# Optimization experiments

Measured on AMD Instinct MI355X. Metric: run time of the kernel, lower is better.

The kernel has to match this reference:

```python
import jax, jax.numpy as jnp
import numpy as np

B, N, D = 4, 1024, 1024      # batch, seq_len, query_dim
H, DH = 16, 64               # heads, dim_head; inner = H*DH = 1024
INNER = H * DH
SCALE = DH ** -0.5


def setup_inputs() -> dict:
    key = jax.random.key(0)
    ks = jax.random.split(key, 8)
    x = jax.random.normal(ks[0], (B, N, D), dtype=jnp.float32)
    rel_pos = jax.random.normal(ks[1], (B * H, N, N), dtype=jnp.float32)
    query_mask = jax.random.randint(ks[2], (B, N), 0, 2).astype(bool)
    context_mask = jax.random.randint(ks[3], (B, N), 0, 2).astype(bool)
    # Linear weights stored (in, out); to_q/to_kv have no bias, to_out has bias.
    Wq = jax.random.normal(ks[4], (D, INNER), dtype=jnp.float32) / np.sqrt(D)
    Wkv = jax.random.normal(ks[5], (D, 2 * INNER), dtype=jnp.float32) / np.sqrt(D)
    Wo = jax.random.normal(ks[6], (INNER, D), dtype=jnp.float32) / np.sqrt(INNER)
    bo = jax.random.normal(ks[7], (D,), dtype=jnp.float32) * 0.01
    return {"x": x, "rel_pos": rel_pos, "query_mask": query_mask,
            "context_mask": context_mask, "Wq": Wq, "Wkv": Wkv, "Wo": Wo, "bo": bo}


def reference(x, rel_pos, query_mask, context_mask, Wq, Wkv, Wo, bo):
    # Self-attention (context = x)
    q = x @ Wq                                 # [B, N, INNER]
    kv = x @ Wkv                               # [B, N, 2*INNER]
    k, v = jnp.split(kv, 2, axis=-1)
    # (b n (h d)) -> (b h n d)
    split_heads = lambda t: t.reshape(B, N, H, DH).transpose(0, 2, 1, 3)
    q, k, v = map(split_heads, (q, k, v))
    sim = jnp.einsum('bhid,bhjd->bhij', q, k) * SCALE
    sim = sim + rel_pos.reshape(B, H, N, N)
    neg = -jnp.finfo(sim.dtype).max
    # query_mask: (b i) -> mask rows; context_mask: (b j) -> mask cols
    sim = jnp.where(query_mask[:, None, :, None], sim, neg)
    sim = jnp.where(context_mask[:, None, None, :], sim, neg)
    attn = jax.nn.softmax(sim, axis=-1)
    out = jnp.einsum('bhij,bhjd->bhid', attn, v)    # [B, H, N, DH]
    out = out.transpose(0, 2, 1, 3).reshape(B, N, INNER)
    return out @ Wo + bo
```

## Files before the change

### kernel.cpp

```cpp
#include <hip/hip_runtime.h>


#define NEGMAX 3.402823466e+38f

typedef short short8 __attribute__((ext_vector_type(8)));
typedef float f32x4 __attribute__((ext_vector_type(4)));

__device__ __forceinline__ unsigned short f2bf(float f) {
  unsigned int u = __float_as_uint(f);
  u += 0x7FFFu + ((u >> 16) & 1u);
  return (unsigned short)(u >> 16);
}

__device__ __forceinline__ void stage16(const void* g, void* lds_base, int lane) {
#if __has_builtin(__builtin_amdgcn_global_load_lds)
  __builtin_amdgcn_global_load_lds(
      (const __attribute__((address_space(1))) unsigned int*)g,
      (__attribute__((address_space(3))) unsigned int*)lds_base, 16, 0, 0);
#else
  *(int4*)((char*)lds_base + lane * 16) = *(const int4*)g;
#endif
}

__global__ void cast_x_k(const float* __restrict__ x, unsigned short* __restrict__ xb) {
  int i = (blockIdx.x * 256 + threadIdx.x) * 4;
  float4 v = *(const float4*)(x + i);
  ushort4 o;
  o.x = f2bf(v.x); o.y = f2bf(v.y); o.z = f2bf(v.z); o.w = f2bf(v.w);
  *(ushort4*)(xb + i) = o;
}

__global__ __launch_bounds__(256) void tcast_k(const float* __restrict__ src, int ldsrc,
                                               unsigned short* __restrict__ dst) {
  __shared__ float T[64][65];
  const int n0 = blockIdx.x * 64, d0 = blockIdx.y * 64;
  const int tx = threadIdx.x & 63, ty = threadIdx.x >> 6;
#pragma unroll
  for (int k = 0; k < 16; ++k) {
    int dl = k * 4 + ty;
    T[dl][tx] = src[(size_t)(d0 + dl) * ldsrc + n0 + tx];
  }
  __syncthreads();
#pragma unroll
  for (int k = 0; k < 16; ++k) {
    int nl = k * 4 + ty;
    dst[(size_t)(n0 + nl) * 1024 + d0 + tx] = f2bf(T[tx][nl]);
  }
}

template <int MODE>
__global__ __launch_bounds__(256) void gemm_bt_k(
    const unsigned short* __restrict__ A, const unsigned short* __restrict__ Bt,
    unsigned short* __restrict__ qws, unsigned short* __restrict__ kws,
    unsigned short* __restrict__ vtws,
    const float* __restrict__ bias, float* __restrict__ Cout) {
  constexpr int K = 1024;
  constexpr int NKB = K / 32;
  __shared__ alignas(16) unsigned short As[128 * 32];
  __shared__ alignas(16) unsigned short Bs[128 * 32];
  const int tid = threadIdx.x;
  const int lane = tid & 63, w = tid >> 6;
  const int quad = lane >> 4, lanelo = lane & 15;
  const int tRow = blockIdx.y * 128, tCol = blockIdx.x * 128;
  const int wr = (w >> 1) * 64, wc = (w & 1) * 64;
  const char* AgB = (const char*)(A + (size_t)tRow * K);
  const char* BgB = (const char*)(Bt + (size_t)tCol * K);
  const int c0 = tid, c1 = tid + 256;
  const size_t a0off = (size_t)(c0 >> 2) * 2048 + (c0 & 3) * 16;
  const size_t a1off = (size_t)(c1 >> 2) * 2048 + (c1 & 3) * 16;
  char* ldsA0 = (char*)As + w * 1024;
  char* ldsA1 = (char*)As + 4096 + w * 1024;
  char* ldsB0 = (char*)Bs + w * 1024;
  char* ldsB1 = (char*)Bs + 4096 + w * 1024;

  f32x4 acc[4][4];
#pragma unroll
  for (int i = 0; i < 4; ++i)
#pragma unroll
    for (int j = 0; j < 4; ++j) acc[i][j] = (f32x4){0.f, 0.f, 0.f, 0.f};

  for (int kb = 0; kb < NKB; ++kb) {
    if (kb) __syncthreads();
    const size_t ko = (size_t)kb * 64;
    stage16(AgB + a0off + ko, ldsA0, lane);
    stage16(AgB + a1off + ko, ldsA1, lane);
    stage16(BgB + a0off + ko, ldsB0, lane);
    stage16(BgB + a1off + ko, ldsB1, lane);
    __syncthreads();

    short8 af[4], bf[4];
#pragma unroll
    for (int i = 0; i < 4; ++i)
      af[i] = *(const short8*)(As + (wr + i * 16 + lanelo) * 32 + quad * 8);
#pragma unroll
    for (int j = 0; j < 4; ++j)
      bf[j] = *(const short8*)(Bs + (wc + j * 16 + lanelo) * 32 + quad * 8);
#pragma unroll
    for (int i = 0; i < 4; ++i)
#pragma unroll
      for (int j = 0; j < 4; ++j)
        acc[i][j] = __builtin_amdgcn_mfma_f32_16x16x32_bf16(af[i], bf[j], acc[i][j], 0, 0, 0);
  }

  if (MODE == 0) {
#pragma unroll
    for (int i = 0; i < 4; ++i) {
      int row = tRow + wr + i * 16 + quad * 4;
      int b_ = row >> 10;
      int npos = row & 1023;
#pragma unroll
      for (int j = 0; j < 4; ++j) {
        int col = tCol + wc + j * 16 + lanelo;
        if (col < 2048) {
          unsigned short* dst = (col < 1024) ? qws : kws;
          int c = col & 1023;
          int hh = c >> 6, dh = c & 63;
          size_t base = ((size_t)(b_ * 16 + hh) * 1024 + npos) * 64 + dh;
#pragma unroll
          for (int r = 0; r < 4; ++r) dst[base + (size_t)r * 64] = f2bf(acc[i][j][r]);
        } else {
          int c = col - 2048;
          ushort4 pk;
          pk.x = f2bf(acc[i][j][0]);
          pk.y = f2bf(acc[i][j][1]);
          pk.z = f2bf(acc[i][j][2]);
          pk.w = f2bf(acc[i][j][3]);
          *(ushort4*)&vtws[((size_t)(b_ * 16 + (c >> 6)) * 64 + (c & 63)) * 1024 + npos] = pk;
        }
      }
    }
  } else {
#pragma unroll
    for (int i = 0; i < 4; ++i) {
      int row = tRow + wr + i * 16 + quad * 4;
#pragma unroll
      for (int j = 0; j < 4; ++j) {
        int col = tCol + wc + j * 16 + lanelo;
        float bv = bias[col];
#pragma unroll
        for (int r = 0; r < 4; ++r)
          Cout[(size_t)(row + r) * 1024 + col] = acc[i][j][r] + bv;
      }
    }
  }
}

__global__ __launch_bounds__(64) void attn_k(
    const unsigned short* __restrict__ q_ws, const unsigned short* __restrict__ k_ws,
    const unsigned short* __restrict__ vt_ws, const float* __restrict__ rel,
    const int* __restrict__ qmask, const int* __restrict__ cmask,
    unsigned short* __restrict__ aout) {
  constexpr float SCALE = 0.125f;
  __shared__ alignas(16) unsigned short Pl[16 * 72];

  const int lane = threadIdx.x;
  const int quad = lane >> 4, lanelo = lane & 15;
  const int bh = blockIdx.y, b_ = bh >> 4, h = bh & 15;
  const int qrow0 = blockIdx.x * 16;

  const unsigned short* qg = q_ws + ((size_t)bh * 1024 + qrow0) * 64;
  short8 qf0 = *(const short8*)(qg + lanelo * 64 + quad * 8);
  short8 qf1 = *(const short8*)(qg + lanelo * 64 + 32 + quad * 8);

  float qmv[4];
#pragma unroll
  for (int r = 0; r < 4; ++r)
    qmv[r] = (qmask[b_ * 1024 + qrow0 + quad * 4 + r] != 0) ? 1.f : 0.f;

  const unsigned short* kg = k_ws + (size_t)bh * 65536;
  const unsigned short* vg = vt_ws + (size_t)bh * 65536;
  const float* relg = rel + ((size_t)bh * 1024 + qrow0) * 1024;
  const int* cmg = cmask + b_ * 1024;

  f32x4 o[4];
#pragma unroll
  for (int g = 0; g < 4; ++g) o[g] = (f32x4){0.f, 0.f, 0.f, 0.f};
  float m_run[4], l_run[4];
#pragma unroll
  for (int r = 0; r < 4; ++r) { m_run[r] = -NEGMAX; l_run[r] = 0.f; }

  float rl[4][4], cmv[4];
#pragma unroll
  for (int r = 0; r < 4; ++r)
#pragma unroll
    for (int c = 0; c < 4; ++c)
      rl[r][c] = relg[(size_t)(quad * 4 + r) * 1024 + c * 16 + lanelo];
#pragma unroll
  for (int c = 0; c < 4; ++c) cmv[c] = (cmg[c * 16 + lanelo] != 0) ? 1.f : 0.f;

  for (int kb = 0; kb < 16; ++kb) {
    const int ko = kb * 64;

    short8 kf0[4], kf1[4];
#pragma unroll
    for (int c = 0; c < 4; ++c) {
      const unsigned short* kr = kg + (size_t)(ko + c * 16 + lanelo) * 64 + quad * 8;
      kf0[c] = *(const short8*)(kr);
      kf1[c] = *(const short8*)(kr + 32);
    }
    short8 vf[4][2];
#pragma unroll
    for (int g = 0; g < 4; ++g)
#pragma unroll
      for (int c2 = 0; c2 < 2; ++c2)
        vf[g][c2] = *(const short8*)(vg + (size_t)(g * 16 + lanelo) * 1024 + ko + c2 * 32 + quad * 8);

    f32x4 s[4];
#pragma unroll
    for (int c = 0; c < 4; ++c) {
      s[c] = (f32x4){0.f, 0.f, 0.f, 0.f};
      s[c] = __builtin_amdgcn_mfma_f32_16x16x32_bf16(qf0, kf0[c], s[c], 0, 0, 0);
      s[c] = __builtin_amdgcn_mfma_f32_16x16x32_bf16(qf1, kf1[c], s[c], 0, 0, 0);
    }

    float rn[4][4], cn[4];
    if (kb + 1 < 16) {
#pragma unroll
      for (int r = 0; r < 4; ++r)
#pragma unroll
        for (int c = 0; c < 4; ++c)
          rn[r][c] = relg[(size_t)(quad * 4 + r) * 1024 + ko + 64 + c * 16 + lanelo];
#pragma unroll
      for (int c = 0; c < 4; ++c) cn[c] = (cmg[ko + 64 + c * 16 + lanelo] != 0) ? 1.f : 0.f;
    }

#pragma unroll
    for (int r = 0; r < 4; ++r) {
      const bool qok = qmv[r] != 0.f;
      float x[4], mloc = -NEGMAX;
#pragma unroll
      for (int c = 0; c < 4; ++c) {
        x[c] = (qok && cmv[c] != 0.f) ? s[c][r] * SCALE + rl[r][c] : -NEGMAX;
        mloc = fmaxf(mloc, x[c]);
      }
      for (int off = 1; off < 16; off <<= 1) mloc = fmaxf(mloc, __shfl_xor(mloc, off));
      float mnew = fmaxf(m_run[r], mloc);
      float alpha = __expf(m_run[r] - mnew);
      m_run[r] = mnew;
      float ps = 0.f;
      unsigned short pb[4];
#pragma unroll
      for (int c = 0; c < 4; ++c) {
        float p = __expf(x[c] - mnew);
        ps += p;
        pb[c] = f2bf(p);
      }
      for (int off = 1; off < 16; off <<= 1) ps += __shfl_xor(ps, off);
      l_run[r] = l_run[r] * alpha + ps;
#pragma unroll
      for (int g = 0; g < 4; ++g) o[g][r] *= alpha;
#pragma unroll
      for (int c = 0; c < 4; ++c) Pl[(quad * 4 + r) * 72 + c * 16 + lanelo] = pb[c];
    }

    if (kb + 1 < 16) {
#pragma unroll
      for (int r = 0; r < 4; ++r)
#pragma unroll
        for (int c = 0; c < 4; ++c) rl[r][c] = rn[r][c];
#pragma unroll
      for (int c = 0; c < 4; ++c) cmv[c] = cn[c];
    }

#pragma unroll
    for (int c2 = 0; c2 < 2; ++c2) {
      short8 pa = *(const short8*)((const char*)Pl + lanelo * 144 + c2 * 64 + quad * 16);
#pragma unroll
      for (int g = 0; g < 4; ++g)
        o[g] = __builtin_amdgcn_mfma_f32_16x16x32_bf16(pa, vf[g][c2], o[g], 0, 0, 0);
    }
  }

#pragma unroll
  for (int r = 0; r < 4; ++r) {
    float inv = 1.f / l_run[r];
    size_t row = (size_t)(b_ * 1024 + qrow0 + quad * 4 + r) * 1024;
#pragma unroll
    for (int g = 0; g < 4; ++g)
      aout[row + h * 64 + g * 16 + lanelo] = f2bf(o[g][r] * inv);
  }
}

extern "C" void kernel_launch(void* const* d_in, const int* in_sizes, int n_in,
                              void* d_out, int out_size, void* d_ws, size_t ws_size,
                              hipStream_t stream) {
  const float* x = (const float*)d_in[0];
  const float* rel = (const float*)d_in[1];
  const int* qmask = (const int*)d_in[2];
  const int* cmask = (const int*)d_in[3];
  const float* Wq = (const float*)d_in[4];
  const float* Wkv = (const float*)d_in[5];
  const float* Wo = (const float*)d_in[6];
  const float* bo = (const float*)d_in[7];
  float* out = (float*)d_out;

  char* ws = (char*)d_ws;
  const size_t MB = 1024 * 1024;
  unsigned short* w3t = (unsigned short*)(ws);
  unsigned short* wot = (unsigned short*)(ws + 6 * MB);
  unsigned short* xb  = (unsigned short*)(ws + 8 * MB);
  unsigned short* qws = (unsigned short*)(ws + 16 * MB);
  unsigned short* kws = (unsigned short*)(ws + 24 * MB);
  unsigned short* vtws = (unsigned short*)(ws + 32 * MB);
  unsigned short* aout = xb;

  cast_x_k<<<4096, 256, 0, stream>>>(x, xb);
  tcast_k<<<dim3(16, 16), 256, 0, stream>>>(Wq, 1024, w3t);
  tcast_k<<<dim3(32, 16), 256, 0, stream>>>(Wkv, 2048, w3t + (size_t)1024 * 1024);
  tcast_k<<<dim3(16, 16), 256, 0, stream>>>(Wo, 1024, wot);
  gemm_bt_k<0><<<dim3(24, 32), 256, 0, stream>>>(xb, w3t, qws, kws, vtws, nullptr, nullptr);
  attn_k<<<dim3(64, 64), 64, 0, stream>>>(qws, kws, vtws, rel, qmask, cmask, aout);
  gemm_bt_k<1><<<dim3(8, 32), 256, 0, stream>>>(aout, wot, nullptr, nullptr, nullptr, bo, out);
}
```

Baseline: 526.6 us.

## Vectorize rel_pos loads via LDS transpose of scores and double-buffer prefetch

The score tile is written to LDS and read back so that each lane owns four contiguous columns. This lets rel_pos and the context mask be loaded as 16-byte vectors instead of scalar strided loads. Those loads are now prefetched two key blocks ahead into a double buffer, the loop is unrolled by two, and the V fragment loads are moved after the score computation. The cost is extra LDS traffic per block, plus the register pressure of two buffers. Correctness relies on the wavefront executing the LDS write and read without an explicit barrier, which holds because each block is a single 64-thread wave.

```diff
diff --git a/kernel.cpp b/kernel.cpp
--- a/kernel.cpp
+++ b/kernel.cpp
@@ -151,6 +151,7 @@
     const int* __restrict__ qmask, const int* __restrict__ cmask,
     unsigned short* __restrict__ aout) {
   constexpr float SCALE = 0.125f;
+  __shared__ alignas(16) float Sl[16 * 70];
   __shared__ alignas(16) unsigned short Pl[16 * 72];
 
   const int lane = threadIdx.x;
@@ -179,15 +180,17 @@
 #pragma unroll
   for (int r = 0; r < 4; ++r) { m_run[r] = -NEGMAX; l_run[r] = 0.f; }
 
-  float rl[4][4], cmv[4];
-#pragma unroll
-  for (int r = 0; r < 4; ++r)
-#pragma unroll
-    for (int c = 0; c < 4; ++c)
-      rl[r][c] = relg[(size_t)(quad * 4 + r) * 1024 + c * 16 + lanelo];
-#pragma unroll
-  for (int c = 0; c < 4; ++c) cmv[c] = (cmg[c * 16 + lanelo] != 0) ? 1.f : 0.f;
-
+  f32x4 R[2][4];
+  int4 C2[2];
+#pragma unroll
+  for (int d = 0; d < 2; ++d) {
+#pragma unroll
+    for (int r = 0; r < 4; ++r)
+      R[d][r] = *(const f32x4*)(relg + (size_t)(quad * 4 + r) * 1024 + d * 64 + 4 * lanelo);
+    C2[d] = *(const int4*)(cmg + d * 64 + 4 * lanelo);
+  }
+
+#pragma unroll 2
   for (int kb = 0; kb < 16; ++kb) {
     const int ko = kb * 64;
 
@@ -198,13 +201,6 @@
       kf0[c] = *(const short8*)(kr);
       kf1[c] = *(const short8*)(kr + 32);
     }
-    short8 vf[4][2];
-#pragma unroll
-    for (int g = 0; g < 4; ++g)
-#pragma unroll
-      for (int c2 = 0; c2 < 2; ++c2)
-        vf[g][c2] = *(const short8*)(vg + (size_t)(g * 16 + lanelo) * 1024 + ko + c2 * 32 + quad * 8);
-
     f32x4 s[4];
 #pragma unroll
     for (int c = 0; c < 4; ++c) {
@@ -213,61 +209,66 @@
       s[c] = __builtin_amdgcn_mfma_f32_16x16x32_bf16(qf1, kf1[c], s[c], 0, 0, 0);
     }
 
-    float rn[4][4], cn[4];
-    if (kb + 1 < 16) {
+#pragma unroll
+    for (int c = 0; c < 4; ++c)
 #pragma unroll
       for (int r = 0; r < 4; ++r)
-#pragma unroll
-        for (int c = 0; c < 4; ++c)
-          rn[r][c] = relg[(size_t)(quad * 4 + r) * 1024 + ko + 64 + c * 16 + lanelo];
-#pragma unroll
-      for (int c = 0; c < 4; ++c) cn[c] = (cmg[ko + 64 + c * 16 + lanelo] != 0) ? 1.f : 0.f;
-    }
+        Sl[(quad * 4 + r) * 70 + c * 16 + lanelo] = s[c][r];
+
+    short8 vf[4][2];
+#pragma unroll
+    for (int g = 0; g < 4; ++g)
+#pragma unroll
+      for (int c2 = 0; c2 < 2; ++c2)
+        vf[g][c2] = *(const short8*)(vg + (size_t)(g * 16 + lanelo) * 1024 + ko + c2 * 32 + quad * 8);
+
+    f32x4 sv[4];
+#pragma unroll
+    for (int r = 0; r < 4; ++r)
+      sv[r] = *(const f32x4*)&Sl[(quad * 4 + r) * 70 + 4 * lanelo];
+
+    const int4 cw = C2[kb & 1];
+    const bool c0 = cw.x != 0, c1 = cw.y != 0, c2m = cw.z != 0, c3 = cw.w != 0;
 
 #pragma unroll
     for (int r = 0; r < 4; ++r) {
       const bool qok = qmv[r] != 0.f;
-      float x[4], mloc = -NEGMAX;
-#pragma unroll
-      for (int c = 0; c < 4; ++c) {
-        x[c] = (qok && cmv[c] != 0.f) ? s[c][r] * SCALE + rl[r][c] : -NEGMAX;
-        mloc = fmaxf(mloc, x[c]);
-      }
+      f32x4 x = sv[r] * SCALE + R[kb & 1][r];
+      x.x = (qok && c0) ? x.x : -NEGMAX;
+      x.y = (qok && c1) ? x.y : -NEGMAX;
+      x.z = (qok && c2m) ? x.z : -NEGMAX;
+      x.w = (qok && c3) ? x.w : -NEGMAX;
+      float mloc = fmaxf(fmaxf(x.x, x.y), fmaxf(x.z, x.w));
       for (int off = 1; off < 16; off <<= 1) mloc = fmaxf(mloc, __shfl_xor(mloc, off));
       float mnew = fmaxf(m_run[r], mloc);
       float alpha = __expf(m_run[r] - mnew);
       m_run[r] = mnew;
-      float ps = 0.f;
-      unsigned short pb[4];
-#pragma unroll
-      for (int c = 0; c < 4; ++c) {
-        float p = __expf(x[c] - mnew);
-        ps += p;
-        pb[c] = f2bf(p);
-      }
+      float p0 = __expf(x.x - mnew), p1 = __expf(x.y - mnew);
+      float p2 = __expf(x.z - mnew), p3 = __expf(x.w - mnew);
+      float ps = (p0 + p1) + (p2 + p3);
       for (int off = 1; off < 16; off <<= 1) ps += __shfl_xor(ps, off);
       l_run[r] = l_run[r] * alpha + ps;
 #pragma unroll
       for (int g = 0; g < 4; ++g) o[g][r] *= alpha;
-#pragma unroll
-      for (int c = 0; c < 4; ++c) Pl[(quad * 4 + r) * 72 + c * 16 + lanelo] = pb[c];
-    }
-
-    if (kb + 1 < 16) {
+      ushort4 pk;
+      pk.x = f2bf(p0); pk.y = f2bf(p1); pk.z = f2bf(p2); pk.w = f2bf(p3);
+      *(ushort4*)&Pl[(quad * 4 + r) * 72 + 4 * lanelo] = pk;
+    }
+
+    {
+      const int kon = (kb + 2 < 16) ? (ko + 128) : 0;
 #pragma unroll
       for (int r = 0; r < 4; ++r)
-#pragma unroll
-        for (int c = 0; c < 4; ++c) rl[r][c] = rn[r][c];
-#pragma unroll
-      for (int c = 0; c < 4; ++c) cmv[c] = cn[c];
-    }
-
-#pragma unroll
-    for (int c2 = 0; c2 < 2; ++c2) {
-      short8 pa = *(const short8*)((const char*)Pl + lanelo * 144 + c2 * 64 + quad * 16);
+        R[kb & 1][r] = *(const f32x4*)(relg + (size_t)(quad * 4 + r) * 1024 + kon + 4 * lanelo);
+      C2[kb & 1] = *(const int4*)(cmg + kon + 4 * lanelo);
+    }
+
+#pragma unroll
+    for (int h2 = 0; h2 < 2; ++h2) {
+      short8 pa = *(const short8*)((const char*)Pl + lanelo * 144 + h2 * 64 + quad * 16);
 #pragma unroll
       for (int g = 0; g < 4; ++g)
-        o[g] = __builtin_amdgcn_mfma_f32_16x16x32_bf16(pa, vf[g][c2], o[g], 0, 0, 0);
+        o[g] = __builtin_amdgcn_mfma_f32_16x16x32_bf16(pa, vf[g][h2], o[g], 0, 0, 0);
     }
   }
 
```

Measured after the change: 604.5 us. 1.15x slower.
